# Optimization experiments

Measured on AMD Instinct MI355X. Metric: run time of the kernel, lower is better.

## Reference

```python
import jax, jax.numpy as jnp
import numpy as np

B, S = 4, 128          # batch, seq
IN, OUT = 1024, 1024   # perfect squares
C = 256                # compressed_feature_dim
K = 4                  # num_monarchs
NI, NO = 32, 32        # sqrt(IN), sqrt(OUT)
D1 = NI * NI * NO      # flat size of M1 per token
D2 = NO * NI * NO      # flat size of M2 per token


def setup_inputs() -> dict:
    key = jax.random.key(0)
    ks = jax.random.split(key, 20)
    s = 0.02
    return {
        "x":   jax.random.normal(ks[0], (B, S, IN), dtype=jnp.float32),
        # compressor: Linear(IN, C)
        "Wc":  jax.random.normal(ks[1], (IN, C), dtype=jnp.float32) * s,
        "bc":  jnp.zeros((C,), dtype=jnp.float32),
        # M1 generators (stacked over K experts): Linear(C,C), SiLU, Linear(C,D1)
        "W1a": jax.random.normal(ks[2], (K, C, C), dtype=jnp.float32) * s,
        "b1a": jnp.zeros((K, C), dtype=jnp.float32),
        "W1b": jax.random.normal(ks[3], (K, C, D1), dtype=jnp.float32) * s,
        "b1b": jax.random.normal(ks[4], (K, D1), dtype=jnp.float32) * s,
        # M2 generators
        "W2a": jax.random.normal(ks[5], (K, C, C), dtype=jnp.float32) * s,
        "b2a": jnp.zeros((K, C), dtype=jnp.float32),
        "W2b": jax.random.normal(ks[6], (K, C, D2), dtype=jnp.float32) * s,
        "b2b": jax.random.normal(ks[7], (K, D2), dtype=jnp.float32) * s,
        # mixer: Linear(C,C), SiLU, Linear(C,K)
        "Wm1": jax.random.normal(ks[8], (C, C), dtype=jnp.float32) * s,
        "bm1": jnp.zeros((C,), dtype=jnp.float32),
        "Wm2": jax.random.normal(ks[9], (C, K), dtype=jnp.float32) * s,
        "bm2": jnp.zeros((K,), dtype=jnp.float32),
        # biasor: Linear(C, OUT)
        "Wb":  jax.random.normal(ks[10], (C, OUT), dtype=jnp.float32) * s,
        "bb":  jnp.zeros((OUT,), dtype=jnp.float32),
        # ratio_gen: Linear(C, 1)
        "Wr":  jax.random.normal(ks[11], (C, 1), dtype=jnp.float32) * s,
        "br":  jnp.ones((1,), dtype=jnp.float32),
    }


def reference(x, Wc, bc, W1a, b1a, W1b, b1b, W2a, b2a, W2b, b2b,
              Wm1, bm1, Wm2, bm2, Wb, bb, Wr, br):
    silu = jax.nn.silu
    # compressor
    c = silu(x @ Wc + bc)                                   # [B,S,C]
    # per-expert hypernetwork generation of flat Monarch factors
    h1 = silu(jnp.einsum('bsc,kcd->kbsd', c, W1a) + b1a[:, None, None, :])
    M1s = jnp.einsum('kbsd,kde->kbse', h1, W1b) + b1b[:, None, None, :]  # [K,B,S,D1]
    h2 = silu(jnp.einsum('bsc,kcd->kbsd', c, W2a) + b2a[:, None, None, :])
    M2s = jnp.einsum('kbsd,kde->kbse', h2, W2b) + b2b[:, None, None, :]  # [K,B,S,D2]
    # softmax mixing coefficients
    coeffs = jax.nn.softmax(silu(c @ Wm1 + bm1) @ Wm2 + bm2, axis=-1)    # [B,S,K]
    M1_flat = jnp.einsum('kbsd,bsk->bsd', M1s, coeffs)      # [B,S,D1]
    M2_flat = jnp.einsum('kbsd,bsk->bsd', M2s, coeffs)      # [B,S,D2]
    # per-token Monarch matmul
    lead = x.shape[:-1]
    M1 = M1_flat.reshape(*lead, NI, NI, NO)
    M2 = M2_flat.reshape(*lead, NO, NI, NO)
    x1 = x.reshape(*lead, NI, NI)                            # [B,S,g=NI,i=NI]
    x1o = jnp.einsum('bsgi,bsgio->bsgo', x1, M1)             # [B,S,NI,NO]
    x2 = jnp.swapaxes(x1o, -1, -2)                           # [B,S,NO,NI]
    x2o = jnp.einsum('bsgi,bsgio->bsgo', x2, M2)             # [B,S,NO,NO]
    y = x2o.reshape(*lead, NO * NO)                          # [B,S,OUT]
    ratio = c @ Wr + br                                      # [B,S,1]
    return y * ratio + (c @ Wb + bb)
```

## Files before the change

kernel.cpp:

```cpp
#include <hip/hip_runtime.h>


typedef __bf16 bf16x8 __attribute__((ext_vector_type(8)));
typedef float  fx4    __attribute__((ext_vector_type(4)));

#define NN 32768

__device__ __forceinline__ unsigned short f2bf(float f) {
  union { float f; unsigned u; } v; v.f = f;
  unsigned r = v.u + 0x7FFFu + ((v.u >> 16) & 1u);
  return (unsigned short)(r >> 16);
}
__device__ __forceinline__ unsigned pk2(float lo, float hi) {
  return (unsigned)f2bf(lo) | ((unsigned)f2bf(hi) << 16);
}
__device__ __forceinline__ float b2f(unsigned short s) {
  union { unsigned u; float f; } v; v.u = ((unsigned)s) << 16; return v.f;
}
__device__ __forceinline__ void up8(uint4 h, float* f) {
  f[0] = b2f((unsigned short)(h.x & 0xFFFF)); f[1] = b2f((unsigned short)(h.x >> 16));
  f[2] = b2f((unsigned short)(h.y & 0xFFFF)); f[3] = b2f((unsigned short)(h.y >> 16));
  f[4] = b2f((unsigned short)(h.z & 0xFFFF)); f[5] = b2f((unsigned short)(h.z >> 16));
  f[6] = b2f((unsigned short)(h.w & 0xFFFF)); f[7] = b2f((unsigned short)(h.w >> 16));
}
__device__ __forceinline__ uint4 scale8(uint4 h, float cv) {
  uint4 u;
  u.x = pk2(b2f((unsigned short)(h.x & 0xFFFF)) * cv, b2f((unsigned short)(h.x >> 16)) * cv);
  u.y = pk2(b2f((unsigned short)(h.y & 0xFFFF)) * cv, b2f((unsigned short)(h.y >> 16)) * cv);
  u.z = pk2(b2f((unsigned short)(h.z & 0xFFFF)) * cv, b2f((unsigned short)(h.z >> 16)) * cv);
  u.w = pk2(b2f((unsigned short)(h.w & 0xFFFF)) * cv, b2f((unsigned short)(h.w >> 16)) * cv);
  return u;
}
__device__ __forceinline__ float silu_f(float x) { return x / (1.f + __expf(-x)); }

__device__ __forceinline__ void gl2lds16(const void* g, void* l) {
  __builtin_amdgcn_global_load_lds(
      (const __attribute__((address_space(1))) unsigned int*)g,
      (__attribute__((address_space(3))) unsigned int*)l, 16, 0, 0);
}

#define MFMA(a, b, c) __builtin_amdgcn_mfma_f32_16x16x32_bf16((a), (b), (c), 0, 0, 0)

__global__ __launch_bounds__(256) void k1_compress(
    const float* __restrict__ x, const float* __restrict__ Wc,
    const float* __restrict__ bc, uint4* __restrict__ c_u4) {
  const int tid = threadIdx.x;
  const int m0 = blockIdx.x * 64, n0 = blockIdx.y * 64;
  __shared__ uint4 As[8 * 64];
  __shared__ uint4 Bs[8 * 65];
  const bf16x8* Af = reinterpret_cast<const bf16x8*>(As);
  const bf16x8* Bf = reinterpret_cast<const bf16x8*>(Bs);
  uint2* Bs2 = reinterpret_cast<uint2*>(Bs);
  const int lane = tid & 63, w = tid >> 6;
  const int q = lane >> 4, rr = lane & 15;
  const int wm = (w >> 1) * 32, wn = (w & 1) * 32;
  const int arun = tid & 7, amb = tid >> 3;
  const int kgrp = tid & 15, colg = tid >> 4;
  fx4 a00 = 0, a01 = 0, a10 = 0, a11 = 0;
  fx4 areg[4], breg[4];

#pragma unroll
  for (int s = 0; s < 2; ++s) {
    const float* src = x + (size_t)(m0 + amb + 32 * s) * 1024 + arun * 8;
    areg[2 * s] = *(const fx4*)src;
    areg[2 * s + 1] = *(const fx4*)(src + 4);
  }
#pragma unroll
  for (int kk = 0; kk < 4; ++kk)
    breg[kk] = *(const fx4*)(Wc + (size_t)(kgrp * 4 + kk) * 256 + n0 + colg * 4);

  for (int kt = 0; kt < 16; ++kt) {
    __syncthreads();
#pragma unroll
    for (int s = 0; s < 2; ++s) {
      uint4 u;
      u.x = pk2(areg[2 * s][0], areg[2 * s][1]);
      u.y = pk2(areg[2 * s][2], areg[2 * s][3]);
      u.z = pk2(areg[2 * s + 1][0], areg[2 * s + 1][1]);
      u.w = pk2(areg[2 * s + 1][2], areg[2 * s + 1][3]);
      As[arun * 64 + amb + 32 * s] = u;
    }
#pragma unroll
    for (int j = 0; j < 4; ++j) {
      uint2 u;
      u.x = pk2(breg[0][j], breg[1][j]);
      u.y = pk2(breg[2][j], breg[3][j]);
      Bs2[(((kgrp >> 1) * 65 + colg * 4 + j) << 1) + (kgrp & 1)] = u;
    }
    __syncthreads();
    if (kt < 15) {
      const int k0 = (kt + 1) * 64;
#pragma unroll
      for (int s = 0; s < 2; ++s) {
        const float* src = x + (size_t)(m0 + amb + 32 * s) * 1024 + k0 + arun * 8;
        areg[2 * s] = *(const fx4*)src;
        areg[2 * s + 1] = *(const fx4*)(src + 4);
      }
#pragma unroll
      for (int kk = 0; kk < 4; ++kk)
        breg[kk] = *(const fx4*)(Wc + (size_t)(k0 + kgrp * 4 + kk) * 256 + n0 + colg * 4);
    }
#pragma unroll
    for (int ks = 0; ks < 2; ++ks) {
      const int roA = (ks * 4 + q) * 64, roB = (ks * 4 + q) * 65;
      bf16x8 fa0 = Af[roA + wm + rr];
      bf16x8 fa1 = Af[roA + wm + 16 + rr];
      bf16x8 fb0 = Bf[roB + wn + rr];
      bf16x8 fb1 = Bf[roB + wn + 16 + rr];
      a00 = MFMA(fa0, fb0, a00); a01 = MFMA(fa0, fb1, a01);
      a10 = MFMA(fa1, fb0, a10); a11 = MFMA(fa1, fb1, a11);
    }
  }
  __syncthreads();
  {
    const int r4 = tid >> 6, m = tid & 63;
    uint4 u; u.x = (r4 == 0) ? 0x3F80u : 0u; u.y = 0; u.z = 0; u.w = 0;
    As[r4 * 64 + m] = u;
    uint4 ub; ub.x = (r4 == 0) ? (unsigned)f2bf(bc[n0 + m]) : 0u;
    ub.y = 0; ub.z = 0; ub.w = 0;
    Bs[r4 * 65 + m] = ub;
  }
  __syncthreads();
  {
    bf16x8 fa0 = Af[q * 64 + wm + rr];
    bf16x8 fa1 = Af[q * 64 + wm + 16 + rr];
    bf16x8 fb0 = Bf[q * 65 + wn + rr];
    bf16x8 fb1 = Bf[q * 65 + wn + 16 + rr];
    a00 = MFMA(fa0, fb0, a00); a01 = MFMA(fa0, fb1, a01);
    a10 = MFMA(fa1, fb0, a10); a11 = MFMA(fa1, fb1, a11);
  }
  unsigned short* c16 = (unsigned short*)c_u4;
#pragma unroll
  for (int fi = 0; fi < 2; ++fi) {
#pragma unroll
    for (int fj = 0; fj < 2; ++fj) {
      fx4 v = (fi == 0) ? (fj == 0 ? a00 : a01) : (fj == 0 ? a10 : a11);
      const int cc = n0 + wn + fj * 16 + rr;
#pragma unroll
      for (int reg = 0; reg < 4; ++reg) {
        const int t = m0 + wm + fi * 16 + q * 4 + reg;
        c16[((size_t)(cc >> 3) * 512 + t) * 8 + (cc & 7)] = f2bf(silu_f(v[reg]));
      }
    }
  }
  if (blockIdx.y == 0) {
    const int r4 = tid >> 6, m = tid & 63;
    uint4 u; u.x = (r4 == 0) ? 0x3F80u : 0u; u.y = 0; u.z = 0; u.w = 0;
    c_u4[(size_t)(32 + r4) * 512 + m0 + m] = u;
  }
}

__global__ __launch_bounds__(256) void k2_hyper(
    const uint4* __restrict__ c_u4,
    const float* __restrict__ W1a, const float* __restrict__ b1a,
    const float* __restrict__ W2a, const float* __restrict__ b2a,
    const float* __restrict__ Wm1, const float* __restrict__ bm1,
    const float* __restrict__ Wb, const float* __restrict__ bb,
    unsigned short* __restrict__ H, float* __restrict__ biasout) {
  const int tid = threadIdx.x;
  const int m0 = blockIdx.x * 64, n0 = blockIdx.y * 64;
  __shared__ uint4 As[2][8 * 64];
  __shared__ uint4 Bs[8 * 65];
  const bf16x8* Bf = reinterpret_cast<const bf16x8*>(Bs);
  uint2* Bs2 = reinterpret_cast<uint2*>(Bs);
  const int lane = tid & 63, w = tid >> 6;
  const int q = lane >> 4, rr = lane & 15;
  const int wm = (w >> 1) * 32, wn = (w & 1) * 32;
  const int kgrp = tid & 15, colg = tid >> 4;

  const float* bbase; const float* biasv; int bstride;
  if (n0 < 1024) {
    const int kx = n0 >> 8;
    bbase = W1a + (size_t)kx * 65536 + (n0 & 255); bstride = 256;
    biasv = b1a + kx * 256 + (n0 & 255);
  } else if (n0 < 2048) {
    const int mm = n0 - 1024; const int kx = mm >> 8;
    bbase = W2a + (size_t)kx * 65536 + (mm & 255); bstride = 256;
    biasv = b2a + kx * 256 + (mm & 255);
  } else if (n0 < 2304) {
    bbase = Wm1 + (n0 - 2048); bstride = 256; biasv = bm1 + (n0 - 2048);
  } else {
    bbase = Wb + (n0 - 2304); bstride = 1024; biasv = bb + (n0 - 2304);
  }

  fx4 a00 = 0, a01 = 0, a10 = 0, a11 = 0;
  fx4 breg[4];
#pragma unroll
  for (int kk = 0; kk < 4; ++kk)
    breg[kk] = *(const fx4*)(bbase + (size_t)(kgrp * 4 + kk) * bstride + colg * 4);
#pragma unroll
  for (int s = 0; s < 2; ++s) {
    const int run = w * 2 + s;
    gl2lds16(c_u4 + (size_t)run * 512 + m0 + lane, (void*)(&As[0][run * 64]));
  }
  int cur = 0;
  for (int kt = 0; kt < 4; ++kt) {
    __syncthreads();
#pragma unroll
    for (int j = 0; j < 4; ++j) {
      uint2 u;
      u.x = pk2(breg[0][j], breg[1][j]);
      u.y = pk2(breg[2][j], breg[3][j]);
      Bs2[(((kgrp >> 1) * 65 + colg * 4 + j) << 1) + (kgrp & 1)] = u;
    }
    __syncthreads();
    if (kt < 3) {
#pragma unroll
      for (int s = 0; s < 2; ++s) {
        const int run = w * 2 + s;
        gl2lds16(c_u4 + (size_t)((kt + 1) * 8 + run) * 512 + m0 + lane,
                 (void*)(&As[cur ^ 1][run * 64]));
      }
#pragma unroll
      for (int kk = 0; kk < 4; ++kk)
        breg[kk] = *(const fx4*)(bbase + (size_t)((kt + 1) * 64 + kgrp * 4 + kk) * bstride + colg * 4);
    }
    const bf16x8* Af = reinterpret_cast<const bf16x8*>(As[cur]);
#pragma unroll
    for (int ks = 0; ks < 2; ++ks) {
      const int roA = (ks * 4 + q) * 64, roB = (ks * 4 + q) * 65;
      bf16x8 fa0 = Af[roA + wm + rr];
      bf16x8 fa1 = Af[roA + wm + 16 + rr];
      bf16x8 fb0 = Bf[roB + wn + rr];
      bf16x8 fb1 = Bf[roB + wn + 16 + rr];
      a00 = MFMA(fa0, fb0, a00); a01 = MFMA(fa0, fb1, a01);
      a10 = MFMA(fa1, fb0, a10); a11 = MFMA(fa1, fb1, a11);
    }
    cur ^= 1;
  }
  __syncthreads();
  {
    gl2lds16(c_u4 + (size_t)(32 + w) * 512 + m0 + lane, (void*)(&As[0][w * 64]));
    const int r4 = tid >> 6, col = tid & 63;
    uint4 ub; ub.x = (r4 == 0) ? (unsigned)f2bf(biasv[col]) : 0u;
    ub.y = 0; ub.z = 0; ub.w = 0;
    Bs[r4 * 65 + col] = ub;
  }
  __syncthreads();
  {
    const bf16x8* Af = reinterpret_cast<const bf16x8*>(As[0]);
    bf16x8 fa0 = Af[q * 64 + wm + rr];
    bf16x8 fa1 = Af[q * 64 + wm + 16 + rr];
    bf16x8 fb0 = Bf[q * 65 + wn + rr];
    bf16x8 fb1 = Bf[q * 65 + wn + 16 + rr];
    a00 = MFMA(fa0, fb0, a00); a01 = MFMA(fa0, fb1, a01);
    a10 = MFMA(fa1, fb0, a10); a11 = MFMA(fa1, fb1, a11);
  }
#pragma unroll
  for (int fi = 0; fi < 2; ++fi) {
#pragma unroll
    for (int fj = 0; fj < 2; ++fj) {
      fx4 v = (fi == 0) ? (fj == 0 ? a00 : a01) : (fj == 0 ? a10 : a11);
      const int cc = n0 + wn + fj * 16 + rr;
#pragma unroll
      for (int reg = 0; reg < 4; ++reg) {
        const int t = m0 + wm + fi * 16 + q * 4 + reg;
        if (n0 < 2304)
          H[(((size_t)(cc >> 3) * 512 + t) << 3) + (cc & 7)] = f2bf(silu_f(v[reg]));
        else
          biasout[(size_t)t * 1024 + (cc - 2304)] = v[reg];
      }
    }
  }
}

__global__ __launch_bounds__(256) void k3_prep(
    const uint4* __restrict__ Hu, const uint4* __restrict__ c_u4,
    const float* __restrict__ Wm2, const float* __restrict__ bm2,
    const float* __restrict__ Wr, const float* __restrict__ br,
    uint4* __restrict__ G1u, uint4* __restrict__ G2u, float* __restrict__ ratio) {
  const int tid = threadIdx.x;
  const int tg = blockIdx.x & 7, dgrp = blockIdx.x >> 3;
  const int t0 = tg * 64;
  __shared__ float sWm2[1024];
  __shared__ float sWr[256];
  __shared__ float part[64][4][4];
  __shared__ float rp[64][4];
  __shared__ float cf[64][4];
  ((fx4*)sWm2)[tid] = ((const fx4*)Wm2)[tid];
  if (tid < 64) ((fx4*)sWr)[tid] = ((const fx4*)Wr)[tid];
  __syncthreads();
  const int tl = tid >> 2, kx = tid & 3;
  {
    float pe0 = 0, pe1 = 0, pe2 = 0, pe3 = 0, pr = 0;
#pragma unroll
    for (int i = 0; i < 8; ++i) {
      uint4 h  = Hu[(size_t)(256 + kx * 8 + i) * 512 + t0 + tl];
      uint4 cu = c_u4[(size_t)(kx * 8 + i) * 512 + t0 + tl];
      float hf[8], cv[8];
      up8(h, hf); up8(cu, cv);
#pragma unroll
      for (int j = 0; j < 8; ++j) {
        const int ch = kx * 64 + i * 8 + j;
        pe0 += hf[j] * sWm2[ch * 4 + 0];
        pe1 += hf[j] * sWm2[ch * 4 + 1];
        pe2 += hf[j] * sWm2[ch * 4 + 2];
        pe3 += hf[j] * sWm2[ch * 4 + 3];
        pr  += cv[j] * sWr[ch];
      }
    }
    part[tl][kx][0] = pe0; part[tl][kx][1] = pe1;
    part[tl][kx][2] = pe2; part[tl][kx][3] = pe3;
    rp[tl][kx] = pr;
  }
  __syncthreads();
  if (tid < 64) {
    float l[4];
#pragma unroll
    for (int e = 0; e < 4; ++e)
      l[e] = part[tid][0][e] + part[tid][1][e] + part[tid][2][e] + part[tid][3][e] + bm2[e];
    float m = fmaxf(fmaxf(l[0], l[1]), fmaxf(l[2], l[3]));
    float e0 = __expf(l[0] - m), e1 = __expf(l[1] - m);
    float e2 = __expf(l[2] - m), e3 = __expf(l[3] - m);
    float den = e0 + e1 + e2 + e3;
    cf[tid][0] = e0 / den; cf[tid][1] = e1 / den;
    cf[tid][2] = e2 / den; cf[tid][3] = e3 / den;
    if (dgrp == 0)
      ratio[t0 + tid] = rp[tid][0] + rp[tid][1] + rp[tid][2] + rp[tid][3] + br[0];
  }
  __syncthreads();
  const int tl2 = tid & 63, sub = tid >> 6;
#pragma unroll
  for (int i = 0; i < 4; ++i) {
    const int dg = dgrp * 16 + sub * 4 + i;
    const float cv = cf[tl2][dg >> 5];
    uint4 h1 = Hu[(size_t)dg * 512 + t0 + tl2];
    G1u[(size_t)dg * 512 + t0 + tl2] = scale8(h1, cv);
    uint4 h2 = Hu[(size_t)(128 + dg) * 512 + t0 + tl2];
    G2u[(size_t)dg * 512 + t0 + tl2] = scale8(h2, cv);
  }
  if (dgrp == 0) {
    if (tid < 64) {
      uint4 u;
      u.x = pk2(cf[tid][0], cf[tid][1]);
      u.y = pk2(cf[tid][2], cf[tid][3]);
      u.z = 0; u.w = 0;
      G1u[(size_t)128 * 512 + t0 + tid] = u;
      G2u[(size_t)128 * 512 + t0 + tid] = u;
    } else {
      const int idx = tid - 64;
      uint4 z; z.x = 0; z.y = 0; z.z = 0; z.w = 0;
      G1u[(size_t)(129 + (idx >> 6)) * 512 + t0 + (idx & 63)] = z;
      G2u[(size_t)(129 + (idx >> 6)) * 512 + t0 + (idx & 63)] = z;
    }
  }
}

__global__ __launch_bounds__(256) void k_biggemm(
    const uint4* __restrict__ Gu, const float* __restrict__ W,
    const float* __restrict__ bvec, unsigned short* __restrict__ Mout) {
  const int tid = threadIdx.x;
  const int p = blockIdx.x;
  const int xcd = p & 7, slot = p >> 3;
  const int m0 = (slot & 3) * 128;
  const int n0 = ((slot >> 2) * 8 + xcd) * 128;
  __shared__ uint4 As[2][8 * 128];
  __shared__ uint4 Bs[8 * 129];
  const bf16x8* Bf = reinterpret_cast<const bf16x8*>(Bs);
  const int lane = tid & 63, w = tid >> 6;
  const int q = lane >> 4, rr = lane & 15;
  const int wm = (w >> 1) * 64, wn = (w & 1) * 64;
  const int colB = tid & 127, half = tid >> 7;
  const int bcg = tid >> 3;
  const int br  = tid & 7;
  const float* wptr = W + n0 + bcg * 4;

  fx4 acc[4][4];
#pragma unroll
  for (int i = 0; i < 4; ++i)
#pragma unroll
    for (int j = 0; j < 4; ++j) acc[i][j] = 0;

  fx4 breg[8];
#pragma unroll
  for (int kk = 0; kk < 8; ++kk)
    breg[kk] = *(const fx4*)(wptr + (size_t)(br * 8 + kk) * NN);
#pragma unroll
  for (int s = 0; s < 4; ++s) {
    const int ch = w * 4 + s, run = ch >> 1, hf = ch & 1;
    gl2lds16(Gu + (size_t)run * 512 + m0 + hf * 64 + lane,
             (void*)(&As[0][run * 128 + hf * 64]));
  }

  int cur = 0;
  for (int kt = 0; kt < 16; ++kt) {
    __syncthreads();
#pragma unroll
    for (int j = 0; j < 4; ++j) {
      uint4 u;
      u.x = pk2(breg[0][j], breg[1][j]);
      u.y = pk2(breg[2][j], breg[3][j]);
      u.z = pk2(breg[4][j], breg[5][j]);
      u.w = pk2(breg[6][j], breg[7][j]);
      Bs[br * 129 + bcg * 4 + j] = u;
    }
    __syncthreads();
    if (kt < 15) {
#pragma unroll
      for (int s = 0; s < 4; ++s) {
        const int ch = w * 4 + s, run = ch >> 1, hf = ch & 1;
        gl2lds16(Gu + (size_t)((kt + 1) * 8 + run) * 512 + m0 + hf * 64 + lane,
                 (void*)(&As[cur ^ 1][run * 128 + hf * 64]));
      }
#pragma unroll
      for (int kk = 0; kk < 8; ++kk)
        breg[kk] = *(const fx4*)(wptr + (size_t)((kt + 1) * 64 + br * 8 + kk) * NN);
    }
    const bf16x8* Afc = reinterpret_cast<const bf16x8*>(As[cur]);
#pragma unroll
    for (int ks = 0; ks < 2; ++ks) {
      bf16x8 a[4], b[4];
      const int roA = (ks * 4 + q) * 128, roB = (ks * 4 + q) * 129;
#pragma unroll
      for (int f = 0; f < 4; ++f) a[f] = Afc[roA + wm + f * 16 + rr];
#pragma unroll
      for (int f = 0; f < 4; ++f) b[f] = Bf[roB + wn + f * 16 + rr];
#pragma unroll
      for (int fi = 0; fi < 4; ++fi)
#pragma unroll
        for (int fj = 0; fj < 4; ++fj) acc[fi][fj] = MFMA(a[fi], b[fj], acc[fi][fj]);
    }
    cur ^= 1;
  }
  __syncthreads();
#pragma unroll
  for (int s = 0; s < 2; ++s) {
    const int ch = w * 2 + s, run = ch >> 1, hf = ch & 1;
    gl2lds16(Gu + (size_t)(128 + run) * 512 + m0 + hf * 64 + lane,
             (void*)(&As[0][run * 128 + hf * 64]));
  }
  if (half == 0) {
#pragma unroll
    for (int r = 0; r < 4; ++r) {
      float v8[8];
#pragma unroll
      for (int j = 0; j < 8; ++j) {
        const int kk = r * 8 + j;
        v8[j] = (kk < 4) ? bvec[(size_t)kk * NN + n0 + colB] : 0.f;
      }
      uint4 u; u.x = pk2(v8[0], v8[1]); u.y = pk2(v8[2], v8[3]);
      u.z = pk2(v8[4], v8[5]); u.w = pk2(v8[6], v8[7]);
      Bs[r * 129 + colB] = u;
    }
  }
  __syncthreads();
  {
    const bf16x8* Af0 = reinterpret_cast<const bf16x8*>(As[0]);
    bf16x8 a[4], b[4];
#pragma unroll
    for (int f = 0; f < 4; ++f) a[f] = Af0[q * 128 + wm + f * 16 + rr];
#pragma unroll
    for (int f = 0; f < 4; ++f) b[f] = Bf[q * 129 + wn + f * 16 + rr];
#pragma unroll
    for (int fi = 0; fi < 4; ++fi)
#pragma unroll
      for (int fj = 0; fj < 4; ++fj) acc[fi][fj] = MFMA(a[fi], b[fj], acc[fi][fj]);
  }
#pragma unroll
  for (int fi = 0; fi < 4; ++fi) {
    const int tb = m0 + wm + fi * 16 + q * 4;
#pragma unroll
    for (int fj = 0; fj < 4; ++fj) {
      const fx4 v = acc[fi][fj];
      const int cc = n0 + wn + fj * 16 + rr;
      const int pc = ((cc >> 5) & 31) * 1024 + (cc >> 10) * 32 + (cc & 31);
#pragma unroll
      for (int reg = 0; reg < 4; ++reg)
        Mout[(size_t)(tb + reg) * NN + pc] = f2bf(v[reg]);
    }
  }
}

__global__ __launch_bounds__(256) void k_monarch1(
    const float* __restrict__ x, const unsigned short* __restrict__ M1p,
    float* __restrict__ XT) {
  const int tp = blockIdx.x, tid = threadIdx.x;
  const int tl = tid >> 7, t2 = tid & 127;
  const int tt = tp * 2 + tl;
  __shared__ float xs[2][1024];
  __shared__ float xo[2][1024];
  {
    const int base = tid * 8;
    *(float4*)&(((float*)xs)[base])     = *(const float4*)&x[(size_t)tp * 2048 + base];
    *(float4*)&(((float*)xs)[base + 4]) = *(const float4*)&x[(size_t)tp * 2048 + base + 4];
  }
  __syncthreads();
  const int g = t2 >> 2, ob = (t2 & 3) * 8;
  const unsigned short* mrow = M1p + (size_t)tt * NN + g * 32 + ob;
  float acc[8] = {0, 0, 0, 0, 0, 0, 0, 0};
#pragma unroll
  for (int i = 0; i < 32; ++i) {
    uint4 mv = *(const uint4*)&mrow[(size_t)i * 1024];
    float mf[8]; up8(mv, mf);
    const float xv = xs[tl][g * 32 + i];
#pragma unroll
    for (int j = 0; j < 8; ++j) acc[j] += xv * mf[j];
  }
#pragma unroll
  for (int j = 0; j < 8; ++j) xo[tl][(ob + j) * 32 + g] = acc[j];
  __syncthreads();
  {
    const int base = tid * 8;
    *(float4*)&XT[(size_t)tp * 2048 + base]     = *(const float4*)&(((float*)xo)[base]);
    *(float4*)&XT[(size_t)tp * 2048 + base + 4] = *(const float4*)&(((float*)xo)[base + 4]);
  }
}

__global__ __launch_bounds__(256) void k_monarch2(
    const unsigned short* __restrict__ M2p, const float* __restrict__ XT,
    const float* __restrict__ biasout, const float* __restrict__ ratio,
    float* __restrict__ out) {
  const int tp = blockIdx.x, tid = threadIdx.x;
  const int tl = tid >> 7, t2 = tid & 127;
  const int tt = tp * 2 + tl;
  __shared__ float xs[2][1024];
  {
    const int base = tid * 8;
    *(float4*)&(((float*)xs)[base])     = *(const float4*)&XT[(size_t)tp * 2048 + base];
    *(float4*)&(((float*)xs)[base + 4]) = *(const float4*)&XT[(size_t)tp * 2048 + base + 4];
  }
  __syncthreads();
  const int g = t2 >> 2, ob = (t2 & 3) * 8;
  const unsigned short* mrow = M2p + (size_t)tt * NN + g * 32 + ob;
  float acc[8] = {0, 0, 0, 0, 0, 0, 0, 0};
#pragma unroll
  for (int i = 0; i < 32; ++i) {
    uint4 mv = *(const uint4*)&mrow[(size_t)i * 1024];
    float mf[8]; up8(mv, mf);
    const float xv = xs[tl][g * 32 + i];
#pragma unroll
    for (int j = 0; j < 8; ++j) acc[j] += xv * mf[j];
  }
  const float r = ratio[tt];
  const int col = g * 32 + ob;
  float4 b0 = *(const float4*)&biasout[(size_t)tt * 1024 + col];
  float4 b1 = *(const float4*)&biasout[(size_t)tt * 1024 + col + 4];
  float4 o0, o1;
  o0.x = acc[0] * r + b0.x; o0.y = acc[1] * r + b0.y;
  o0.z = acc[2] * r + b0.z; o0.w = acc[3] * r + b0.w;
  o1.x = acc[4] * r + b1.x; o1.y = acc[5] * r + b1.y;
  o1.z = acc[6] * r + b1.z; o1.w = acc[7] * r + b1.w;
  *(float4*)&out[(size_t)tt * 1024 + col]     = o0;
  *(float4*)&out[(size_t)tt * 1024 + col + 4] = o1;
}

extern "C" void kernel_launch(void* const* d_in, const int* in_sizes, int n_in,
                              void* d_out, int out_size, void* d_ws, size_t ws_size,
                              hipStream_t stream) {
  (void)in_sizes; (void)n_in; (void)out_size; (void)ws_size;
  const float* x   = (const float*)d_in[0];
  const float* Wc  = (const float*)d_in[1];
  const float* bc  = (const float*)d_in[2];
  const float* W1a = (const float*)d_in[3];
  const float* b1a = (const float*)d_in[4];
  const float* W1b = (const float*)d_in[5];
  const float* b1b = (const float*)d_in[6];
  const float* W2a = (const float*)d_in[7];
  const float* b2a = (const float*)d_in[8];
  const float* W2b = (const float*)d_in[9];
  const float* b2b = (const float*)d_in[10];
  const float* Wm1 = (const float*)d_in[11];
  const float* bm1 = (const float*)d_in[12];
  const float* Wm2 = (const float*)d_in[13];
  const float* bm2 = (const float*)d_in[14];
  const float* Wb  = (const float*)d_in[15];
  const float* bb  = (const float*)d_in[16];
  const float* Wr  = (const float*)d_in[17];
  const float* br  = (const float*)d_in[18];
  float* out = (float*)d_out;

  char* ws = (char*)d_ws;
  uint4* c_u4            = (uint4*)(ws + 0);
  unsigned short* H      = (unsigned short*)(ws + 294912);
  float* biasout         = (float*)(ws + 2654208);
  uint4* G1u             = (uint4*)(ws + 4751360);
  uint4* G2u             = (uint4*)(ws + 5832704);
  float* ratio           = (float*)(ws + 6914048);
  float* XT              = (float*)(ws + 6918144);
  unsigned short* M      = (unsigned short*)(ws + 9015296);

  k1_compress<<<dim3(8, 4), 256, 0, stream>>>(x, Wc, bc, c_u4);
  k2_hyper<<<dim3(8, 52), 256, 0, stream>>>(c_u4, W1a, b1a, W2a, b2a, Wm1, bm1,
                                            Wb, bb, H, biasout);
  k3_prep<<<64, 256, 0, stream>>>((const uint4*)H, c_u4, Wm2, bm2, Wr, br,
                                  G1u, G2u, ratio);
  k_biggemm<<<1024, 256, 0, stream>>>(G1u, W1b, b1b, M);
  k_monarch1<<<256, 256, 0, stream>>>(x, M, XT);
  k_biggemm<<<1024, 256, 0, stream>>>(G2u, W2b, b2b, M);
  k_monarch2<<<256, 256, 0, stream>>>(M, XT, biasout, ratio, out);
}
```

Measured before the change: 501.4 us.

## Load GEMM A-operand straight to registers, double-buffer B tile, split monarch K-loop

The big hypernetwork GEMM no longer stages the A operand (G) through LDS. Each wave loads its A fragments from global memory into registers with a one-step-ahead prefetch. The B tile converted from fp32 weights is now double-buffered in LDS, which removes one barrier per k-iteration. The fp32-to-bf16 conversion switches to the native __bf16 cast, and the monarch kernels use one block per token with the 32-row reduction split across two half-blocks, combined through LDS, doubling the grid. In exchange this adds register pressure, makes A reads uncoalesced from global memory, and adds an extra LDS reduction step.

```diff
diff --git a/kernel.cpp b/kernel.cpp
--- a/kernel.cpp
+++ b/kernel.cpp
@@ -2,17 +2,17 @@
 
 
 typedef __bf16 bf16x8 __attribute__((ext_vector_type(8)));
+typedef __bf16 bf16x2 __attribute__((ext_vector_type(2)));
 typedef float  fx4    __attribute__((ext_vector_type(4)));
 
 #define NN 32768
 
 __device__ __forceinline__ unsigned short f2bf(float f) {
-  union { float f; unsigned u; } v; v.f = f;
-  unsigned r = v.u + 0x7FFFu + ((v.u >> 16) & 1u);
-  return (unsigned short)(r >> 16);
+  union { __bf16 b; unsigned short u; } c; c.b = (__bf16)f; return c.u;
 }
 __device__ __forceinline__ unsigned pk2(float lo, float hi) {
-  return (unsigned)f2bf(lo) | ((unsigned)f2bf(hi) << 16);
+  bf16x2 v; v[0] = (__bf16)lo; v[1] = (__bf16)hi;
+  union { bf16x2 v; unsigned u; } c; c.v = v; return c.u;
 }
 __device__ __forceinline__ float b2f(unsigned short s) {
   union { unsigned u; float f; } v; v.u = ((unsigned)s) << 16; return v.f;
@@ -354,16 +354,14 @@
   const int xcd = p & 7, slot = p >> 3;
   const int m0 = (slot & 3) * 128;
   const int n0 = ((slot >> 2) * 8 + xcd) * 128;
-  __shared__ uint4 As[2][8 * 128];
-  __shared__ uint4 Bs[8 * 129];
-  const bf16x8* Bf = reinterpret_cast<const bf16x8*>(Bs);
+  __shared__ uint4 Bs[2][8 * 129];
   const int lane = tid & 63, w = tid >> 6;
   const int q = lane >> 4, rr = lane & 15;
   const int wm = (w >> 1) * 64, wn = (w & 1) * 64;
-  const int colB = tid & 127, half = tid >> 7;
   const int bcg = tid >> 3;
   const int br  = tid & 7;
   const float* wptr = W + n0 + bcg * 4;
+  const uint4* aptr = Gu + m0 + wm + rr;
 
   fx4 acc[4][4];
 #pragma unroll
@@ -372,89 +370,92 @@
     for (int j = 0; j < 4; ++j) acc[i][j] = 0;
 
   fx4 breg[8];
+  uint4 a_cur[4], a_nxt[4];
 #pragma unroll
   for (int kk = 0; kk < 8; ++kk)
     breg[kk] = *(const fx4*)(wptr + (size_t)(br * 8 + kk) * NN);
 #pragma unroll
-  for (int s = 0; s < 4; ++s) {
-    const int ch = w * 4 + s, run = ch >> 1, hf = ch & 1;
-    gl2lds16(Gu + (size_t)run * 512 + m0 + hf * 64 + lane,
-             (void*)(&As[0][run * 128 + hf * 64]));
-  }
-
-  int cur = 0;
+  for (int j = 0; j < 4; ++j) {
+    uint4 u;
+    u.x = pk2(breg[0][j], breg[1][j]); u.y = pk2(breg[2][j], breg[3][j]);
+    u.z = pk2(breg[4][j], breg[5][j]); u.w = pk2(breg[6][j], breg[7][j]);
+    Bs[0][br * 129 + bcg * 4 + j] = u;
+  }
+#pragma unroll
+  for (int kk = 0; kk < 8; ++kk)
+    breg[kk] = *(const fx4*)(wptr + (size_t)(64 + br * 8 + kk) * NN);
+#pragma unroll
+  for (int f = 0; f < 4; ++f) a_cur[f] = aptr[(size_t)q * 512 + f * 16];
+  __syncthreads();
+
   for (int kt = 0; kt < 16; ++kt) {
+    const int cur = kt & 1;
+    const bf16x8* Bf = reinterpret_cast<const bf16x8*>(Bs[cur]);
+    if (kt < 15) {
+#pragma unroll
+      for (int j = 0; j < 4; ++j) {
+        uint4 u;
+        u.x = pk2(breg[0][j], breg[1][j]); u.y = pk2(breg[2][j], breg[3][j]);
+        u.z = pk2(breg[4][j], breg[5][j]); u.w = pk2(breg[6][j], breg[7][j]);
+        Bs[cur ^ 1][br * 129 + bcg * 4 + j] = u;
+      }
+      if (kt < 14) {
+#pragma unroll
+        for (int kk = 0; kk < 8; ++kk)
+          breg[kk] = *(const fx4*)(wptr + (size_t)((kt + 2) * 64 + br * 8 + kk) * NN);
+      }
+    }
+#pragma unroll
+    for (int ks = 0; ks < 2; ++ks) {
+      if (kt < 15 || ks < 1) {
+        const int nk8 = (ks == 0) ? (kt * 8 + 4 + q) : ((kt + 1) * 8 + q);
+#pragma unroll
+        for (int f = 0; f < 4; ++f) a_nxt[f] = aptr[(size_t)nk8 * 512 + f * 16];
+      }
+      bf16x8 b[4];
+      const int roB = (ks * 4 + q) * 129;
+#pragma unroll
+      for (int f = 0; f < 4; ++f) b[f] = Bf[roB + wn + f * 16 + rr];
+#pragma unroll
+      for (int fi = 0; fi < 4; ++fi) {
+        bf16x8 af = *reinterpret_cast<bf16x8*>(&a_cur[fi]);
+#pragma unroll
+        for (int fj = 0; fj < 4; ++fj) acc[fi][fj] = MFMA(af, b[fj], acc[fi][fj]);
+      }
+#pragma unroll
+      for (int f = 0; f < 4; ++f) a_cur[f] = a_nxt[f];
+    }
     __syncthreads();
-#pragma unroll
-    for (int j = 0; j < 4; ++j) {
-      uint4 u;
-      u.x = pk2(breg[0][j], breg[1][j]);
-      u.y = pk2(breg[2][j], breg[3][j]);
-      u.z = pk2(breg[4][j], breg[5][j]);
-      u.w = pk2(breg[6][j], breg[7][j]);
-      Bs[br * 129 + bcg * 4 + j] = u;
+  }
+  {
+#pragma unroll
+    for (int f = 0; f < 4; ++f) a_cur[f] = aptr[(size_t)(128 + q) * 512 + f * 16];
+    const int colB = tid & 127, half = tid >> 7;
+    if (half == 0) {
+#pragma unroll
+      for (int r = 0; r < 4; ++r) {
+        float v8[8];
+#pragma unroll
+        for (int j = 0; j < 8; ++j) {
+          const int kk = r * 8 + j;
+          v8[j] = (kk < 4) ? bvec[(size_t)kk * NN + n0 + colB] : 0.f;
+        }
+        uint4 u; u.x = pk2(v8[0], v8[1]); u.y = pk2(v8[2], v8[3]);
+        u.z = pk2(v8[4], v8[5]); u.w = pk2(v8[6], v8[7]);
+        Bs[0][r * 129 + colB] = u;
+      }
     }
     __syncthreads();
-    if (kt < 15) {
-#pragma unroll
-      for (int s = 0; s < 4; ++s) {
-        const int ch = w * 4 + s, run = ch >> 1, hf = ch & 1;
-        gl2lds16(Gu + (size_t)((kt + 1) * 8 + run) * 512 + m0 + hf * 64 + lane,
-                 (void*)(&As[cur ^ 1][run * 128 + hf * 64]));
-      }
-#pragma unroll
-      for (int kk = 0; kk < 8; ++kk)
-        breg[kk] = *(const fx4*)(wptr + (size_t)((kt + 1) * 64 + br * 8 + kk) * NN);
-    }
-    const bf16x8* Afc = reinterpret_cast<const bf16x8*>(As[cur]);
-#pragma unroll
-    for (int ks = 0; ks < 2; ++ks) {
-      bf16x8 a[4], b[4];
-      const int roA = (ks * 4 + q) * 128, roB = (ks * 4 + q) * 129;
-#pragma unroll
-      for (int f = 0; f < 4; ++f) a[f] = Afc[roA + wm + f * 16 + rr];
-#pragma unroll
-      for (int f = 0; f < 4; ++f) b[f] = Bf[roB + wn + f * 16 + rr];
-#pragma unroll
-      for (int fi = 0; fi < 4; ++fi)
-#pragma unroll
-        for (int fj = 0; fj < 4; ++fj) acc[fi][fj] = MFMA(a[fi], b[fj], acc[fi][fj]);
-    }
-    cur ^= 1;
-  }
-  __syncthreads();
-#pragma unroll
-  for (int s = 0; s < 2; ++s) {
-    const int ch = w * 2 + s, run = ch >> 1, hf = ch & 1;
-    gl2lds16(Gu + (size_t)(128 + run) * 512 + m0 + hf * 64 + lane,
-             (void*)(&As[0][run * 128 + hf * 64]));
-  }
-  if (half == 0) {
-#pragma unroll
-    for (int r = 0; r < 4; ++r) {
-      float v8[8];
-#pragma unroll
-      for (int j = 0; j < 8; ++j) {
-        const int kk = r * 8 + j;
-        v8[j] = (kk < 4) ? bvec[(size_t)kk * NN + n0 + colB] : 0.f;
-      }
-      uint4 u; u.x = pk2(v8[0], v8[1]); u.y = pk2(v8[2], v8[3]);
-      u.z = pk2(v8[4], v8[5]); u.w = pk2(v8[6], v8[7]);
-      Bs[r * 129 + colB] = u;
-    }
-  }
-  __syncthreads();
-  {
-    const bf16x8* Af0 = reinterpret_cast<const bf16x8*>(As[0]);
-    bf16x8 a[4], b[4];
-#pragma unroll
-    for (int f = 0; f < 4; ++f) a[f] = Af0[q * 128 + wm + f * 16 + rr];
-#pragma unroll
-    for (int f = 0; f < 4; ++f) b[f] = Bf[q * 129 + wn + f * 16 + rr];
-#pragma unroll
-    for (int fi = 0; fi < 4; ++fi)
-#pragma unroll
-      for (int fj = 0; fj < 4; ++fj) acc[fi][fj] = MFMA(a[fi], b[fj], acc[fi][fj]);
+    const bf16x8* Bf0 = reinterpret_cast<const bf16x8*>(Bs[0]);
+    bf16x8 b[4];
+#pragma unroll
+    for (int f = 0; f < 4; ++f) b[f] = Bf0[q * 129 + wn + f * 16 + rr];
+#pragma unroll
+    for (int fi = 0; fi < 4; ++fi) {
+      bf16x8 af = *reinterpret_cast<bf16x8*>(&a_cur[fi]);
+#pragma unroll
+      for (int fj = 0; fj < 4; ++fj) acc[fi][fj] = MFMA(af, b[fj], acc[fi][fj]);
+    }
   }
 #pragma unroll
   for (int fi = 0; fi < 4; ++fi) {
@@ -474,35 +475,34 @@
 __global__ __launch_bounds__(256) void k_monarch1(
     const float* __restrict__ x, const unsigned short* __restrict__ M1p,
     float* __restrict__ XT) {
-  const int tp = blockIdx.x, tid = threadIdx.x;
-  const int tl = tid >> 7, t2 = tid & 127;
-  const int tt = tp * 2 + tl;
-  __shared__ float xs[2][1024];
+  const int tt = blockIdx.x, tid = threadIdx.x;
+  const int h = tid >> 7, t2 = tid & 127;
+  __shared__ float xs[1024];
   __shared__ float xo[2][1024];
-  {
-    const int base = tid * 8;
-    *(float4*)&(((float*)xs)[base])     = *(const float4*)&x[(size_t)tp * 2048 + base];
-    *(float4*)&(((float*)xs)[base + 4]) = *(const float4*)&x[(size_t)tp * 2048 + base + 4];
-  }
+  *(float4*)&xs[tid * 4] = *(const float4*)&x[(size_t)tt * 1024 + tid * 4];
   __syncthreads();
   const int g = t2 >> 2, ob = (t2 & 3) * 8;
-  const unsigned short* mrow = M1p + (size_t)tt * NN + g * 32 + ob;
+  const unsigned short* mrow =
+      M1p + (size_t)tt * NN + (size_t)h * 16 * 1024 + g * 32 + ob;
   float acc[8] = {0, 0, 0, 0, 0, 0, 0, 0};
 #pragma unroll
-  for (int i = 0; i < 32; ++i) {
+  for (int i = 0; i < 16; ++i) {
     uint4 mv = *(const uint4*)&mrow[(size_t)i * 1024];
     float mf[8]; up8(mv, mf);
-    const float xv = xs[tl][g * 32 + i];
+    const float xv = xs[g * 32 + h * 16 + i];
 #pragma unroll
     for (int j = 0; j < 8; ++j) acc[j] += xv * mf[j];
   }
 #pragma unroll
-  for (int j = 0; j < 8; ++j) xo[tl][(ob + j) * 32 + g] = acc[j];
-  __syncthreads();
-  {
-    const int base = tid * 8;
-    *(float4*)&XT[(size_t)tp * 2048 + base]     = *(const float4*)&(((float*)xo)[base]);
-    *(float4*)&XT[(size_t)tp * 2048 + base + 4] = *(const float4*)&(((float*)xo)[base + 4]);
+  for (int j = 0; j < 8; ++j) xo[h][(ob + j) * 32 + g] = acc[j];
+  __syncthreads();
+  {
+    const int base = tid * 4;
+    float4 v0 = *(const float4*)&xo[0][base];
+    float4 v1 = *(const float4*)&xo[1][base];
+    float4 o; o.x = v0.x + v1.x; o.y = v0.y + v1.y;
+    o.z = v0.z + v1.z; o.w = v0.w + v1.w;
+    *(float4*)&XT[(size_t)tt * 1024 + base] = o;
   }
 }
 
@@ -510,38 +510,38 @@
     const unsigned short* __restrict__ M2p, const float* __restrict__ XT,
     const float* __restrict__ biasout, const float* __restrict__ ratio,
     float* __restrict__ out) {
-  const int tp = blockIdx.x, tid = threadIdx.x;
-  const int tl = tid >> 7, t2 = tid & 127;
-  const int tt = tp * 2 + tl;
-  __shared__ float xs[2][1024];
-  {
-    const int base = tid * 8;
-    *(float4*)&(((float*)xs)[base])     = *(const float4*)&XT[(size_t)tp * 2048 + base];
-    *(float4*)&(((float*)xs)[base + 4]) = *(const float4*)&XT[(size_t)tp * 2048 + base + 4];
-  }
+  const int tt = blockIdx.x, tid = threadIdx.x;
+  const int h = tid >> 7, t2 = tid & 127;
+  __shared__ float xs[1024];
+  __shared__ float xo[2][1024];
+  *(float4*)&xs[tid * 4] = *(const float4*)&XT[(size_t)tt * 1024 + tid * 4];
   __syncthreads();
   const int g = t2 >> 2, ob = (t2 & 3) * 8;
-  const unsigned short* mrow = M2p + (size_t)tt * NN + g * 32 + ob;
+  const unsigned short* mrow =
+      M2p + (size_t)tt * NN + (size_t)h * 16 * 1024 + g * 32 + ob;
   float acc[8] = {0, 0, 0, 0, 0, 0, 0, 0};
 #pragma unroll
-  for (int i = 0; i < 32; ++i) {
+  for (int i = 0; i < 16; ++i) {
     uint4 mv = *(const uint4*)&mrow[(size_t)i * 1024];
     float mf[8]; up8(mv, mf);
-    const float xv = xs[tl][g * 32 + i];
+    const float xv = xs[g * 32 + h * 16 + i];
 #pragma unroll
     for (int j = 0; j < 8; ++j) acc[j] += xv * mf[j];
   }
-  const float r = ratio[tt];
-  const int col = g * 32 + ob;
-  float4 b0 = *(const float4*)&biasout[(size_t)tt * 1024 + col];
-  float4 b1 = *(const float4*)&biasout[(size_t)tt * 1024 + col + 4];
-  float4 o0, o1;
-  o0.x = acc[0] * r + b0.x; o0.y = acc[1] * r + b0.y;
-  o0.z = acc[2] * r + b0.z; o0.w = acc[3] * r + b0.w;
-  o1.x = acc[4] * r + b1.x; o1.y = acc[5] * r + b1.y;
-  o1.z = acc[6] * r + b1.z; o1.w = acc[7] * r + b1.w;
-  *(float4*)&out[(size_t)tt * 1024 + col]     = o0;
-  *(float4*)&out[(size_t)tt * 1024 + col + 4] = o1;
+#pragma unroll
+  for (int j = 0; j < 8; ++j) xo[h][g * 32 + ob + j] = acc[j];
+  __syncthreads();
+  {
+    const float r = ratio[tt];
+    const int base = tid * 4;
+    float4 v0 = *(const float4*)&xo[0][base];
+    float4 v1 = *(const float4*)&xo[1][base];
+    float4 bo = *(const float4*)&biasout[(size_t)tt * 1024 + base];
+    float4 o;
+    o.x = (v0.x + v1.x) * r + bo.x; o.y = (v0.y + v1.y) * r + bo.y;
+    o.z = (v0.z + v1.z) * r + bo.z; o.w = (v0.w + v1.w) * r + bo.w;
+    *(float4*)&out[(size_t)tt * 1024 + base] = o;
+  }
 }
 
 extern "C" void kernel_launch(void* const* d_in, const int* in_sizes, int n_in,
@@ -585,7 +585,7 @@
   k3_prep<<<64, 256, 0, stream>>>((const uint4*)H, c_u4, Wm2, bm2, Wr, br,
                                   G1u, G2u, ratio);
   k_biggemm<<<1024, 256, 0, stream>>>(G1u, W1b, b1b, M);
-  k_monarch1<<<256, 256, 0, stream>>>(x, M, XT);
+  k_monarch1<<<512, 256, 0, stream>>>(x, M, XT);
   k_biggemm<<<1024, 256, 0, stream>>>(G2u, W2b, b2b, M);
-  k_monarch2<<<256, 256, 0, stream>>>(M, XT, biasout, ratio, out);
-}
+  k_monarch2<<<512, 256, 0, stream>>>(M, XT, biasout, ratio, out);
+}
```

New measurement: 471.2 us. 6.0% less time.
